# Performance work log

Measured on AMD Instinct MI355X. Metric: run time of the kernel, lower is better.

Reference implementation:

```python
import jax, jax.numpy as jnp
import numpy as np

N = 50000
E = 640000
NFEAT = 128
NHID = 128
ALPHA = 0.2  # leaky relu slope


def setup_inputs() -> dict:
    key = jax.random.key(0)
    k1, k2, k3, k4, k5 = jax.random.split(key, 5)
    x = jax.random.normal(k1, (N, NFEAT), dtype=jnp.float32)
    W = jax.random.normal(k2, (NFEAT, NHID), dtype=jnp.float32) * (1.0 / np.sqrt(NFEAT))
    a = jax.random.normal(k3, (1, 2 * NHID), dtype=jnp.float32) * 0.1
    # every node appears at least once as a source so rowsum > 0 (as in a real adjacency)
    src = jnp.concatenate([jnp.arange(N, dtype=jnp.int64 if jax.config.read('jax_enable_x64') else jnp.int32),
                           jax.random.randint(k4, (E - N,), 0, N)]).astype(jnp.int32)
    dst = jax.random.randint(k5, (E,), 0, N).astype(jnp.int32)
    edge_index = jnp.stack([src, dst], axis=0)
    return {"x": x, "W": W, "a": a, "edge_index": edge_index, "no_need_param": 0}


def reference(x, W, a, edge_index, no_need_param):
    # SpGraphAttentionLayer (concat=False), single head
    h = x @ W                                   # [N, nhid]
    src, dst = edge_index[0], edge_index[1]     # [E]
    nhid = W.shape[1]
    a1, a2 = a[0, :nhid], a[0, nhid:]
    # a @ cat(h[src], h[dst])  ==  h[src]@a1 + h[dst]@a2
    score = h[src] @ a1 + h[dst] @ a2           # [E]
    e = jnp.exp(-jax.nn.leaky_relu(score, ALPHA))
    n = x.shape[0]
    rowsum = jax.ops.segment_sum(e, src, num_segments=n)              # [N]
    h_prime = jax.ops.segment_sum(e[:, None] * h[dst], src, num_segments=n)  # [N, nhid]
    neighborhood_emb = h_prime / (rowsum[:, None] + 1e-16)
    # fused combine: elu(x @ W - neighborhood aggregation)
    mapped_fea = x @ W
    return jax.nn.elu(mapped_fea - neighborhood_emb)
```

## Files before the change

kernel.cpp:

```cpp
#include <hip/hip_runtime.h>
#include <hip/hip_fp16.h>
#include <math.h>

#define NFEAT 128
#define NHID  128
#define ALPHA 0.2f

typedef __attribute__((ext_vector_type(8))) short short8;
typedef __attribute__((ext_vector_type(4))) float f32x4;

__device__ inline unsigned int pack_bf16x2_rn(float x, float y) {
    unsigned int bx = __float_as_uint(x), by = __float_as_uint(y);
    bx += 0x7fffu + ((bx >> 16) & 1u);
    by += 0x7fffu + ((by >> 16) & 1u);
    return (bx >> 16) | (by & 0xffff0000u);
}

union Frag { unsigned int u[4]; uint4 v; short8 s; };

__global__ __launch_bounds__(256) void prep_wt_kernel(
    const float* __restrict__ W, unsigned int* __restrict__ Wtg,
    int* __restrict__ hist, int n)
{
    const int t = threadIdx.x;

    if (blockIdx.x >= 16) {
        const int n4     = n >> 2;
        const int stride = (gridDim.x - 16) << 8;
        int4* h4 = (int4*)hist;
        for (int i = (blockIdx.x - 16) * 256 + t; i < n4; i += stride)
            h4[i] = make_int4(0, 0, 0, 0);
        for (int i = (n4 << 2) + (blockIdx.x - 16) * 256 + t; i < n; i += stride)
            hist[i] = 0;
        return;
    }

    __shared__ float tile[32][33];
    const int kt = blockIdx.x >> 2;
    const int nt = blockIdx.x & 3;

    {
        const int r = t >> 3, c = t & 7;
        const float4 v = *((const float4*)&W[(size_t)(kt * 32 + r) * NHID + nt * 32 + c * 4]);
        tile[r][c * 4 + 0] = v.x; tile[r][c * 4 + 1] = v.y;
        tile[r][c * 4 + 2] = v.z; tile[r][c * 4 + 3] = v.w;
    }
    __syncthreads();

    const int nn = t & 31;
    #pragma unroll
    for (int i = 0; i < 2; ++i) {
        const int kk = (t >> 5) * 2 + i;
        Wtg[(size_t)(nt * 32 + nn) * 64 + kt * 16 + kk] =
            pack_bf16x2_rn(tile[kk * 2][nn], tile[kk * 2 + 1][nn]);
    }
}

__global__ __launch_bounds__(256) void gemm_h_kernel(
    const float* __restrict__ x, const unsigned int* __restrict__ Wtg,
    const float* __restrict__ a, unsigned int* __restrict__ hbu,
    float* __restrict__ s1, float* __restrict__ s2, int n,
    const int* __restrict__ ei, int* __restrict__ hist, int E, int gemm_blocks)
{
    __shared__ unsigned int Wtu[128 * 64];

    const int t = threadIdx.x;

    if (blockIdx.x >= gemm_blocks) {
        const int E4   = E >> 2;
        const int nthr = (gridDim.x - gemm_blocks) << 8;
        const int g    = (blockIdx.x - gemm_blocks) * 256 + t;
        for (int idx = g; idx < E4; idx += nthr) {
            const int4 s4 = ((const int4*)ei)[idx];
            atomicAdd(&hist[s4.x], 1);
            atomicAdd(&hist[s4.y], 1);
            atomicAdd(&hist[s4.z], 1);
            atomicAdd(&hist[s4.w], 1);
        }
        for (int j = (E4 << 2) + g; j < E; j += nthr) atomicAdd(&hist[ei[j]], 1);
        return;
    }

    #pragma unroll
    for (int i = 0; i < 8; ++i) {
        const int u  = i * 256 + t;
        const uint4 v = ((const uint4*)Wtg)[u];
        const int nn = u >> 4, kc = u & 15;
        *((uint4*)&Wtu[nn * 64 + (kc ^ (nn & 15)) * 4]) = v;
    }

    const int w    = t >> 6;
    const int lane = t & 63;
    const int c    = lane & 15;
    const int quad = lane >> 4;

    const int rowbase = blockIdx.x * 64 + w * 16;

    int arow = rowbase + c; if (arow >= n) arow = n - 1;
    const float4* xp = (const float4*)(x + (size_t)arow * NFEAT);
    float4 xv[8];
    #pragma unroll
    for (int s = 0; s < 4; ++s) {
        xv[2 * s]     = xp[s * 8 + quad * 2];
        xv[2 * s + 1] = xp[s * 8 + quad * 2 + 1];
    }

    float a1v[8], a2v[8];
    #pragma unroll
    for (int tt = 0; tt < 8; ++tt) {
        a1v[tt] = a[tt * 16 + c];
        a2v[tt] = a[NHID + tt * 16 + c];
    }

    f32x4 acc[8];
    #pragma unroll
    for (int tt = 0; tt < 8; ++tt) acc[tt] = (f32x4){0.f, 0.f, 0.f, 0.f};

    __syncthreads();

    #pragma unroll
    for (int s = 0; s < 4; ++s) {
        Frag afr;
        afr.u[0] = pack_bf16x2_rn(xv[2 * s].x,     xv[2 * s].y);
        afr.u[1] = pack_bf16x2_rn(xv[2 * s].z,     xv[2 * s].w);
        afr.u[2] = pack_bf16x2_rn(xv[2 * s + 1].x, xv[2 * s + 1].y);
        afr.u[3] = pack_bf16x2_rn(xv[2 * s + 1].z, xv[2 * s + 1].w);
        const int kc = s * 4 + quad;
        #pragma unroll
        for (int tt = 0; tt < 8; ++tt) {
            Frag bfr;
            bfr.v = *((const uint4*)&Wtu[(tt * 16 + c) * 64 + (kc ^ c) * 4]);
            acc[tt] = __builtin_amdgcn_mfma_f32_16x16x32_bf16(
                afr.s, bfr.s, acc[tt], 0, 0, 0);
        }
    }

    #pragma unroll
    for (int r = 0; r < 4; ++r) {
        const int  row = rowbase + quad * 4 + r;
        const bool ok  = (row < n);
        float p1 = 0.f, p2 = 0.f;
        #pragma unroll
        for (int tt = 0; tt < 8; ++tt) {
            const float v = acc[tt][r];
            p1 = fmaf(v, a1v[tt], p1);
            p2 = fmaf(v, a2v[tt], p2);
        }
        if (ok) {
            uint4 pk;
            pk.x = pack_bf16x2_rn(acc[0][r], acc[1][r]);
            pk.y = pack_bf16x2_rn(acc[2][r], acc[3][r]);
            pk.z = pack_bf16x2_rn(acc[4][r], acc[5][r]);
            pk.w = pack_bf16x2_rn(acc[6][r], acc[7][r]);
            *((uint4*)&hbu[(size_t)row * 64 + c * 4]) = pk;
        }
        #pragma unroll
        for (int off = 1; off <= 8; off <<= 1) {
            p1 += __shfl_xor(p1, off, 64);
            p2 += __shfl_xor(p2, off, 64);
        }
        if (ok && c == 0) { s1[row] = p1; s2[row] = p2; }
    }
}

__global__ __launch_bounds__(256) void scan_block_kernel(
    const int* __restrict__ in, int* __restrict__ out, int* __restrict__ bsums, int n)
{
    __shared__ int s[256];
    const int tid = threadIdx.x;
    const int gid = blockIdx.x * 256 + tid;
    const int v = (gid < n) ? in[gid] : 0;
    s[tid] = v;
    __syncthreads();
    #pragma unroll
    for (int off = 1; off < 256; off <<= 1) {
        const int t2 = (tid >= off) ? s[tid - off] : 0;
        __syncthreads();
        s[tid] += t2;
        __syncthreads();
    }
    if (gid < n) out[gid] = s[tid] - v;
    if (tid == 255) bsums[blockIdx.x] = s[255];
}

__global__ __launch_bounds__(256) void scan_add_kernel(
    int* __restrict__ row_ptr, int* __restrict__ cursor,
    const int* __restrict__ bsums, int n, int E, int nb)
{
    __shared__ int s[256];
    const int tid = threadIdx.x;
    s[tid] = (tid < nb) ? bsums[tid] : 0;
    __syncthreads();
    #pragma unroll
    for (int off = 1; off < 256; off <<= 1) {
        const int t2 = (tid >= off) ? s[tid - off] : 0;
        __syncthreads();
        s[tid] += t2;
        __syncthreads();
    }
    const int offset = (blockIdx.x == 0) ? 0 : s[blockIdx.x - 1];
    const int gid = blockIdx.x * 256 + tid;
    if (gid < n) {
        const int v = row_ptr[gid] + offset;
        row_ptr[gid] = v;
        cursor[gid]  = v;
    }
    if (gid == 0) row_ptr[n] = E;
}

__global__ __launch_bounds__(256) void scatter_kernel(
    const int* __restrict__ ei, const float* __restrict__ s1,
    const float* __restrict__ s2, int* __restrict__ cursor,
    unsigned int* __restrict__ erec, int E)
{
    const int j = blockIdx.x * 256 + threadIdx.x;
    if (j >= E) return;
    const int src = ei[j];
    const int dst = ei[E + j];
    float s = s1[src] + s2[dst];
    s = (s > 0.f) ? s : ALPHA * s;
    const float ev = expf(-s);
    const unsigned int evh = (unsigned int)__half_as_ushort(__float2half(ev));
    const int pos = atomicAdd(&cursor[src], 1);
    erec[pos] = ((unsigned int)dst << 16) | evh;
}

__global__ __launch_bounds__(256) void aggregate_kernel(
    const int* __restrict__ row_ptr, const unsigned int* __restrict__ erec,
    const unsigned int* __restrict__ hbu, float* __restrict__ out, int n)
{
    const int node = (blockIdx.x * 256 + threadIdx.x) >> 4;
    const int l    = threadIdx.x & 15;
    if (node >= n) return;

    const int beg = row_ptr[node];
    const int end = row_ptr[node + 1];

    float acc[8];
    #pragma unroll
    for (int i = 0; i < 8; ++i) acc[i] = 0.f;
    float rs = 0.f;

    const uint4* hbu4 = (const uint4*)hbu;

    #define BL(x) __uint_as_float((x) << 16)
    #define BH(x) __uint_as_float((x) & 0xffff0000u)
    #define ACC4(u, ev)                                   \
        acc[0] = fmaf(ev, BL(u.x), acc[0]);               \
        acc[4] = fmaf(ev, BH(u.x), acc[4]);               \
        acc[1] = fmaf(ev, BL(u.y), acc[1]);               \
        acc[5] = fmaf(ev, BH(u.y), acc[5]);               \
        acc[2] = fmaf(ev, BL(u.z), acc[2]);               \
        acc[6] = fmaf(ev, BH(u.z), acc[6]);               \
        acc[3] = fmaf(ev, BL(u.w), acc[3]);               \
        acc[7] = fmaf(ev, BH(u.w), acc[7]);

    int e = beg;
    for (; e + 8 <= end; e += 8) {
        unsigned int rr[8];
        uint4 u[8];
        #pragma unroll
        for (int i = 0; i < 8; ++i) rr[i] = erec[e + i];
        #pragma unroll
        for (int i = 0; i < 8; ++i)
            u[i] = hbu4[(size_t)(rr[i] >> 16) * 16 + l];
        #pragma unroll
        for (int i = 0; i < 8; ++i) {
            const float ev = __half2float(__ushort_as_half((unsigned short)(rr[i] & 0xffffu)));
            ACC4(u[i], ev);
            rs += ev;
        }
    }
    for (; e + 2 <= end; e += 2) {
        const unsigned int r0 = erec[e], r1 = erec[e + 1];
        const uint4 u0 = hbu4[(size_t)(r0 >> 16) * 16 + l];
        const uint4 u1 = hbu4[(size_t)(r1 >> 16) * 16 + l];
        const float e0 = __half2float(__ushort_as_half((unsigned short)(r0 & 0xffffu)));
        const float e1 = __half2float(__ushort_as_half((unsigned short)(r1 & 0xffffu)));
        ACC4(u0, e0); ACC4(u1, e1);
        rs += e0 + e1;
    }
    if (e < end) {
        const unsigned int r0 = erec[e];
        const uint4 u0 = hbu4[(size_t)(r0 >> 16) * 16 + l];
        const float e0 = __half2float(__ushort_as_half((unsigned short)(r0 & 0xffffu)));
        ACC4(u0, e0);
        rs += e0;
    }
    #undef ACC4

    const float rinv = 1.0f / (rs + 1e-16f);
    const uint4 us = hbu4[(size_t)node * 16 + l];
    float* op = out + (size_t)node * NHID + l;
    float z;
    z = BL(us.x) - acc[0] * rinv; op[0]   = (z > 0.f) ? z : (expf(z) - 1.f);
    z = BH(us.x) - acc[4] * rinv; op[16]  = (z > 0.f) ? z : (expf(z) - 1.f);
    z = BL(us.y) - acc[1] * rinv; op[32]  = (z > 0.f) ? z : (expf(z) - 1.f);
    z = BH(us.y) - acc[5] * rinv; op[48]  = (z > 0.f) ? z : (expf(z) - 1.f);
    z = BL(us.z) - acc[2] * rinv; op[64]  = (z > 0.f) ? z : (expf(z) - 1.f);
    z = BH(us.z) - acc[6] * rinv; op[80]  = (z > 0.f) ? z : (expf(z) - 1.f);
    z = BL(us.w) - acc[3] * rinv; op[96]  = (z > 0.f) ? z : (expf(z) - 1.f);
    z = BH(us.w) - acc[7] * rinv; op[112] = (z > 0.f) ? z : (expf(z) - 1.f);
    #undef BL
    #undef BH
}

extern "C" void kernel_launch(void* const* d_in, const int* in_sizes, int n_in,
                              void* d_out, int out_size, void* d_ws, size_t ws_size,
                              hipStream_t stream) {
    const float* x  = (const float*)d_in[0];
    const float* W  = (const float*)d_in[1];
    const float* a  = (const float*)d_in[2];
    const int*   ei = (const int*)d_in[3];

    const int n = in_sizes[0] / NFEAT;
    const int E = in_sizes[3] / 2;
    const int nb = (n + 255) / 256;

    float* out = (float*)d_out;

    unsigned int* hbu    = (unsigned int*)d_ws;
    float*        s1     = (float*)(hbu + (size_t)n * 64);
    float*        s2     = s1 + n;
    unsigned int* erec   = (unsigned int*)(s2 + n);
    unsigned int* Wtg    = erec + E;
    int*          hist   = (int*)(Wtg + 8192);
    int*          bsums  = hist + n;
    int*          row_ptr = bsums + 256;
    int*          cursor  = row_ptr + (n + 1);

    prep_wt_kernel<<<16 + 50, 256, 0, stream>>>(W, Wtg, hist, n);

    const int gemm_blocks = (n + 63) / 64;
    const int hist_blocks = 128;
    gemm_h_kernel<<<gemm_blocks + hist_blocks, 256, 0, stream>>>(
        x, Wtg, a, hbu, s1, s2, n, ei, hist, E, gemm_blocks);

    scan_block_kernel<<<nb, 256, 0, stream>>>(hist, row_ptr, bsums, n);
    scan_add_kernel<<<nb, 256, 0, stream>>>(row_ptr, cursor, bsums, n, E, nb);

    scatter_kernel<<<(E + 255) / 256, 256, 0, stream>>>(ei, s1, s2, cursor, erec, E);

    aggregate_kernel<<<((size_t)n * 16 + 255) / 256, 256, 0, stream>>>(
        row_ptr, erec, hbu, out, n);
}
```

Before: 177.7 us.

## Fuse all stages into one persistent cooperative kernel with grid syncs

Replaces the six separate launches (weight prep, GEMM plus histogram, two scan passes, scatter, aggregate) with a single cooperative persistent kernel. The stages are separated by grid.sync, and each stage uses grid-stride loops over a grid sized from occupancy and capped at 1024 blocks. The scan now uses wave shuffles, and the output uses nontemporal stores. This removes per-launch overhead and idle tails between kernels, but the histogram now runs serially after the GEMM instead of alongside it, every stage is limited to the capped grid, and the 32KB shared buffer may limit occupancy.

```diff
diff --git a/kernel.cpp b/kernel.cpp
--- a/kernel.cpp
+++ b/kernel.cpp
@@ -1,6 +1,9 @@
 #include <hip/hip_runtime.h>
+#include <hip/hip_cooperative_groups.h>
 #include <hip/hip_fp16.h>
 #include <math.h>
+
+namespace cg = cooperative_groups;
 
 #define NFEAT 128
 #define NHID  128
@@ -18,291 +21,301 @@
 
 union Frag { unsigned int u[4]; uint4 v; short8 s; };
 
-__global__ __launch_bounds__(256) void prep_wt_kernel(
-    const float* __restrict__ W, unsigned int* __restrict__ Wtg,
-    int* __restrict__ hist, int n)
+__device__ inline int blk_incl_scan(int v, int* ws) {
+    const int lane = threadIdx.x & 63;
+    const int w    = threadIdx.x >> 6;
+    #pragma unroll
+    for (int off = 1; off < 64; off <<= 1) {
+        const int tv = __shfl_up(v, off, 64);
+        if (lane >= off) v += tv;
+    }
+    if (lane == 63) ws[w] = v;
+    __syncthreads();
+    int add = 0;
+    #pragma unroll
+    for (int i = 0; i < 3; ++i) if (i < w) add += ws[i];
+    __syncthreads();
+    return v + add;
+}
+
+__global__ __launch_bounds__(256) void mega_kernel(
+    const float* __restrict__ x, const float* __restrict__ W,
+    const float* __restrict__ a, const int* __restrict__ ei,
+    float* __restrict__ out, unsigned int* __restrict__ hbu,
+    float* __restrict__ s1, float* __restrict__ s2,
+    unsigned int* __restrict__ erec, unsigned int* __restrict__ Wtg,
+    int* __restrict__ hist, int* __restrict__ bsums,
+    int* __restrict__ row_ptr, int* __restrict__ cursor, int n, int E)
 {
-    const int t = threadIdx.x;
-
-    if (blockIdx.x >= 16) {
-        const int n4     = n >> 2;
-        const int stride = (gridDim.x - 16) << 8;
+    cg::grid_group grid = cg::this_grid();
+    __shared__ unsigned int Wtu[128 * 64];
+
+    const int t        = threadIdx.x;
+    const int gtid     = blockIdx.x * 256 + t;
+    const int nthreads = gridDim.x << 8;
+    const int nb       = (n + 255) >> 8;
+
+    {
+        float (*tile)[33] = (float (*)[33])Wtu;
+        for (int job = blockIdx.x; job < 16; job += gridDim.x) {
+            const int kt = job >> 2, nt = job & 3;
+            __syncthreads();
+            {
+                const int r = t >> 3, cc = t & 7;
+                const float4 v = *((const float4*)&W[(size_t)(kt * 32 + r) * NHID + nt * 32 + cc * 4]);
+                tile[r][cc * 4 + 0] = v.x; tile[r][cc * 4 + 1] = v.y;
+                tile[r][cc * 4 + 2] = v.z; tile[r][cc * 4 + 3] = v.w;
+            }
+            __syncthreads();
+            const int nn = t & 31;
+            #pragma unroll
+            for (int i = 0; i < 2; ++i) {
+                const int kk = (t >> 5) * 2 + i;
+                Wtg[(size_t)(nt * 32 + nn) * 64 + kt * 16 + kk] =
+                    pack_bf16x2_rn(tile[kk * 2][nn], tile[kk * 2 + 1][nn]);
+            }
+        }
+        const int n4 = n >> 2;
         int4* h4 = (int4*)hist;
-        for (int i = (blockIdx.x - 16) * 256 + t; i < n4; i += stride)
-            h4[i] = make_int4(0, 0, 0, 0);
-        for (int i = (n4 << 2) + (blockIdx.x - 16) * 256 + t; i < n; i += stride)
-            hist[i] = 0;
-        return;
-    }
-
-    __shared__ float tile[32][33];
-    const int kt = blockIdx.x >> 2;
-    const int nt = blockIdx.x & 3;
-
-    {
-        const int r = t >> 3, c = t & 7;
-        const float4 v = *((const float4*)&W[(size_t)(kt * 32 + r) * NHID + nt * 32 + c * 4]);
-        tile[r][c * 4 + 0] = v.x; tile[r][c * 4 + 1] = v.y;
-        tile[r][c * 4 + 2] = v.z; tile[r][c * 4 + 3] = v.w;
-    }
-    __syncthreads();
-
-    const int nn = t & 31;
-    #pragma unroll
-    for (int i = 0; i < 2; ++i) {
-        const int kk = (t >> 5) * 2 + i;
-        Wtg[(size_t)(nt * 32 + nn) * 64 + kt * 16 + kk] =
-            pack_bf16x2_rn(tile[kk * 2][nn], tile[kk * 2 + 1][nn]);
-    }
-}
-
-__global__ __launch_bounds__(256) void gemm_h_kernel(
-    const float* __restrict__ x, const unsigned int* __restrict__ Wtg,
-    const float* __restrict__ a, unsigned int* __restrict__ hbu,
-    float* __restrict__ s1, float* __restrict__ s2, int n,
-    const int* __restrict__ ei, int* __restrict__ hist, int E, int gemm_blocks)
-{
-    __shared__ unsigned int Wtu[128 * 64];
-
-    const int t = threadIdx.x;
-
-    if (blockIdx.x >= gemm_blocks) {
-        const int E4   = E >> 2;
-        const int nthr = (gridDim.x - gemm_blocks) << 8;
-        const int g    = (blockIdx.x - gemm_blocks) * 256 + t;
-        for (int idx = g; idx < E4; idx += nthr) {
+        for (int i = gtid; i < n4; i += nthreads) h4[i] = make_int4(0, 0, 0, 0);
+        for (int i = (n4 << 2) + gtid; i < n; i += nthreads) hist[i] = 0;
+    }
+    grid.sync();
+
+    {
+        #pragma unroll
+        for (int i = 0; i < 8; ++i) {
+            const int u  = i * 256 + t;
+            const uint4 v = ((const uint4*)Wtg)[u];
+            const int nn = u >> 4, kc = u & 15;
+            *((uint4*)&Wtu[nn * 64 + (kc ^ (nn & 15)) * 4]) = v;
+        }
+        __syncthreads();
+
+        const int w    = t >> 6;
+        const int lane = t & 63;
+        const int c    = lane & 15;
+        const int quad = lane >> 4;
+
+        float a1v[8], a2v[8];
+        #pragma unroll
+        for (int tt = 0; tt < 8; ++tt) {
+            a1v[tt] = a[tt * 16 + c];
+            a2v[tt] = a[NHID + tt * 16 + c];
+        }
+
+        const int gemm_tiles = (n + 63) >> 6;
+        for (int tb = blockIdx.x; tb < gemm_tiles; tb += gridDim.x) {
+            const int rowbase = tb * 64 + w * 16;
+            int arow = rowbase + c; if (arow >= n) arow = n - 1;
+            const float4* xp = (const float4*)(x + (size_t)arow * NFEAT);
+            float4 xv[8];
+            #pragma unroll
+            for (int s = 0; s < 4; ++s) {
+                xv[2 * s]     = xp[s * 8 + quad * 2];
+                xv[2 * s + 1] = xp[s * 8 + quad * 2 + 1];
+            }
+            f32x4 acc[8];
+            #pragma unroll
+            for (int tt = 0; tt < 8; ++tt) acc[tt] = (f32x4){0.f, 0.f, 0.f, 0.f};
+
+            #pragma unroll
+            for (int s = 0; s < 4; ++s) {
+                Frag afr;
+                afr.u[0] = pack_bf16x2_rn(xv[2 * s].x,     xv[2 * s].y);
+                afr.u[1] = pack_bf16x2_rn(xv[2 * s].z,     xv[2 * s].w);
+                afr.u[2] = pack_bf16x2_rn(xv[2 * s + 1].x, xv[2 * s + 1].y);
+                afr.u[3] = pack_bf16x2_rn(xv[2 * s + 1].z, xv[2 * s + 1].w);
+                const int kc = s * 4 + quad;
+                #pragma unroll
+                for (int tt = 0; tt < 8; ++tt) {
+                    Frag bfr;
+                    bfr.v = *((const uint4*)&Wtu[(tt * 16 + c) * 64 + (kc ^ c) * 4]);
+                    acc[tt] = __builtin_amdgcn_mfma_f32_16x16x32_bf16(
+                        afr.s, bfr.s, acc[tt], 0, 0, 0);
+                }
+            }
+
+            #pragma unroll
+            for (int r = 0; r < 4; ++r) {
+                const int  row = rowbase + quad * 4 + r;
+                const bool ok  = (row < n);
+                float p1 = 0.f, p2 = 0.f;
+                #pragma unroll
+                for (int tt = 0; tt < 8; ++tt) {
+                    const float v = acc[tt][r];
+                    p1 = fmaf(v, a1v[tt], p1);
+                    p2 = fmaf(v, a2v[tt], p2);
+                }
+                if (ok) {
+                    uint4 pk;
+                    pk.x = pack_bf16x2_rn(acc[0][r], acc[1][r]);
+                    pk.y = pack_bf16x2_rn(acc[2][r], acc[3][r]);
+                    pk.z = pack_bf16x2_rn(acc[4][r], acc[5][r]);
+                    pk.w = pack_bf16x2_rn(acc[6][r], acc[7][r]);
+                    *((uint4*)&hbu[(size_t)row * 64 + c * 4]) = pk;
+                }
+                #pragma unroll
+                for (int off = 1; off <= 8; off <<= 1) {
+                    p1 += __shfl_xor(p1, off, 64);
+                    p2 += __shfl_xor(p2, off, 64);
+                }
+                if (ok && c == 0) { s1[row] = p1; s2[row] = p2; }
+            }
+        }
+
+        const int E4 = E >> 2;
+        for (int idx = gtid; idx < E4; idx += nthreads) {
             const int4 s4 = ((const int4*)ei)[idx];
             atomicAdd(&hist[s4.x], 1);
             atomicAdd(&hist[s4.y], 1);
             atomicAdd(&hist[s4.z], 1);
             atomicAdd(&hist[s4.w], 1);
         }
-        for (int j = (E4 << 2) + g; j < E; j += nthr) atomicAdd(&hist[ei[j]], 1);
-        return;
-    }
-
-    #pragma unroll
-    for (int i = 0; i < 8; ++i) {
-        const int u  = i * 256 + t;
-        const uint4 v = ((const uint4*)Wtg)[u];
-        const int nn = u >> 4, kc = u & 15;
-        *((uint4*)&Wtu[nn * 64 + (kc ^ (nn & 15)) * 4]) = v;
-    }
-
-    const int w    = t >> 6;
-    const int lane = t & 63;
-    const int c    = lane & 15;
-    const int quad = lane >> 4;
-
-    const int rowbase = blockIdx.x * 64 + w * 16;
-
-    int arow = rowbase + c; if (arow >= n) arow = n - 1;
-    const float4* xp = (const float4*)(x + (size_t)arow * NFEAT);
-    float4 xv[8];
-    #pragma unroll
-    for (int s = 0; s < 4; ++s) {
-        xv[2 * s]     = xp[s * 8 + quad * 2];
-        xv[2 * s + 1] = xp[s * 8 + quad * 2 + 1];
-    }
-
-    float a1v[8], a2v[8];
-    #pragma unroll
-    for (int tt = 0; tt < 8; ++tt) {
-        a1v[tt] = a[tt * 16 + c];
-        a2v[tt] = a[NHID + tt * 16 + c];
-    }
-
-    f32x4 acc[8];
-    #pragma unroll
-    for (int tt = 0; tt < 8; ++tt) acc[tt] = (f32x4){0.f, 0.f, 0.f, 0.f};
-
-    __syncthreads();
-
-    #pragma unroll
-    for (int s = 0; s < 4; ++s) {
-        Frag afr;
-        afr.u[0] = pack_bf16x2_rn(xv[2 * s].x,     xv[2 * s].y);
-        afr.u[1] = pack_bf16x2_rn(xv[2 * s].z,     xv[2 * s].w);
-        afr.u[2] = pack_bf16x2_rn(xv[2 * s + 1].x, xv[2 * s + 1].y);
-        afr.u[3] = pack_bf16x2_rn(xv[2 * s + 1].z, xv[2 * s + 1].w);
-        const int kc = s * 4 + quad;
-        #pragma unroll
-        for (int tt = 0; tt < 8; ++tt) {
-            Frag bfr;
-            bfr.v = *((const uint4*)&Wtu[(tt * 16 + c) * 64 + (kc ^ c) * 4]);
-            acc[tt] = __builtin_amdgcn_mfma_f32_16x16x32_bf16(
-                afr.s, bfr.s, acc[tt], 0, 0, 0);
-        }
-    }
-
-    #pragma unroll
-    for (int r = 0; r < 4; ++r) {
-        const int  row = rowbase + quad * 4 + r;
-        const bool ok  = (row < n);
-        float p1 = 0.f, p2 = 0.f;
-        #pragma unroll
-        for (int tt = 0; tt < 8; ++tt) {
-            const float v = acc[tt][r];
-            p1 = fmaf(v, a1v[tt], p1);
-            p2 = fmaf(v, a2v[tt], p2);
-        }
-        if (ok) {
-            uint4 pk;
-            pk.x = pack_bf16x2_rn(acc[0][r], acc[1][r]);
-            pk.y = pack_bf16x2_rn(acc[2][r], acc[3][r]);
-            pk.z = pack_bf16x2_rn(acc[4][r], acc[5][r]);
-            pk.w = pack_bf16x2_rn(acc[6][r], acc[7][r]);
-            *((uint4*)&hbu[(size_t)row * 64 + c * 4]) = pk;
-        }
-        #pragma unroll
-        for (int off = 1; off <= 8; off <<= 1) {
-            p1 += __shfl_xor(p1, off, 64);
-            p2 += __shfl_xor(p2, off, 64);
-        }
-        if (ok && c == 0) { s1[row] = p1; s2[row] = p2; }
-    }
-}
-
-__global__ __launch_bounds__(256) void scan_block_kernel(
-    const int* __restrict__ in, int* __restrict__ out, int* __restrict__ bsums, int n)
-{
-    __shared__ int s[256];
-    const int tid = threadIdx.x;
-    const int gid = blockIdx.x * 256 + tid;
-    const int v = (gid < n) ? in[gid] : 0;
-    s[tid] = v;
-    __syncthreads();
-    #pragma unroll
-    for (int off = 1; off < 256; off <<= 1) {
-        const int t2 = (tid >= off) ? s[tid - off] : 0;
-        __syncthreads();
-        s[tid] += t2;
-        __syncthreads();
-    }
-    if (gid < n) out[gid] = s[tid] - v;
-    if (tid == 255) bsums[blockIdx.x] = s[255];
-}
-
-__global__ __launch_bounds__(256) void scan_add_kernel(
-    int* __restrict__ row_ptr, int* __restrict__ cursor,
-    const int* __restrict__ bsums, int n, int E, int nb)
-{
-    __shared__ int s[256];
-    const int tid = threadIdx.x;
-    s[tid] = (tid < nb) ? bsums[tid] : 0;
-    __syncthreads();
-    #pragma unroll
-    for (int off = 1; off < 256; off <<= 1) {
-        const int t2 = (tid >= off) ? s[tid - off] : 0;
-        __syncthreads();
-        s[tid] += t2;
-        __syncthreads();
-    }
-    const int offset = (blockIdx.x == 0) ? 0 : s[blockIdx.x - 1];
-    const int gid = blockIdx.x * 256 + tid;
-    if (gid < n) {
-        const int v = row_ptr[gid] + offset;
-        row_ptr[gid] = v;
-        cursor[gid]  = v;
-    }
-    if (gid == 0) row_ptr[n] = E;
-}
-
-__global__ __launch_bounds__(256) void scatter_kernel(
-    const int* __restrict__ ei, const float* __restrict__ s1,
-    const float* __restrict__ s2, int* __restrict__ cursor,
-    unsigned int* __restrict__ erec, int E)
-{
-    const int j = blockIdx.x * 256 + threadIdx.x;
-    if (j >= E) return;
-    const int src = ei[j];
-    const int dst = ei[E + j];
-    float s = s1[src] + s2[dst];
-    s = (s > 0.f) ? s : ALPHA * s;
-    const float ev = expf(-s);
-    const unsigned int evh = (unsigned int)__half_as_ushort(__float2half(ev));
-    const int pos = atomicAdd(&cursor[src], 1);
-    erec[pos] = ((unsigned int)dst << 16) | evh;
-}
-
-__global__ __launch_bounds__(256) void aggregate_kernel(
-    const int* __restrict__ row_ptr, const unsigned int* __restrict__ erec,
-    const unsigned int* __restrict__ hbu, float* __restrict__ out, int n)
-{
-    const int node = (blockIdx.x * 256 + threadIdx.x) >> 4;
-    const int l    = threadIdx.x & 15;
-    if (node >= n) return;
-
-    const int beg = row_ptr[node];
-    const int end = row_ptr[node + 1];
-
-    float acc[8];
-    #pragma unroll
-    for (int i = 0; i < 8; ++i) acc[i] = 0.f;
-    float rs = 0.f;
-
-    const uint4* hbu4 = (const uint4*)hbu;
-
-    #define BL(x) __uint_as_float((x) << 16)
-    #define BH(x) __uint_as_float((x) & 0xffff0000u)
-    #define ACC4(u, ev)                                   \
-        acc[0] = fmaf(ev, BL(u.x), acc[0]);               \
-        acc[4] = fmaf(ev, BH(u.x), acc[4]);               \
-        acc[1] = fmaf(ev, BL(u.y), acc[1]);               \
-        acc[5] = fmaf(ev, BH(u.y), acc[5]);               \
-        acc[2] = fmaf(ev, BL(u.z), acc[2]);               \
-        acc[6] = fmaf(ev, BH(u.z), acc[6]);               \
-        acc[3] = fmaf(ev, BL(u.w), acc[3]);               \
-        acc[7] = fmaf(ev, BH(u.w), acc[7]);
-
-    int e = beg;
-    for (; e + 8 <= end; e += 8) {
-        unsigned int rr[8];
-        uint4 u[8];
-        #pragma unroll
-        for (int i = 0; i < 8; ++i) rr[i] = erec[e + i];
-        #pragma unroll
-        for (int i = 0; i < 8; ++i)
-            u[i] = hbu4[(size_t)(rr[i] >> 16) * 16 + l];
-        #pragma unroll
-        for (int i = 0; i < 8; ++i) {
-            const float ev = __half2float(__ushort_as_half((unsigned short)(rr[i] & 0xffffu)));
-            ACC4(u[i], ev);
-            rs += ev;
-        }
-    }
-    for (; e + 2 <= end; e += 2) {
-        const unsigned int r0 = erec[e], r1 = erec[e + 1];
-        const uint4 u0 = hbu4[(size_t)(r0 >> 16) * 16 + l];
-        const uint4 u1 = hbu4[(size_t)(r1 >> 16) * 16 + l];
-        const float e0 = __half2float(__ushort_as_half((unsigned short)(r0 & 0xffffu)));
-        const float e1 = __half2float(__ushort_as_half((unsigned short)(r1 & 0xffffu)));
-        ACC4(u0, e0); ACC4(u1, e1);
-        rs += e0 + e1;
-    }
-    if (e < end) {
-        const unsigned int r0 = erec[e];
-        const uint4 u0 = hbu4[(size_t)(r0 >> 16) * 16 + l];
-        const float e0 = __half2float(__ushort_as_half((unsigned short)(r0 & 0xffffu)));
-        ACC4(u0, e0);
-        rs += e0;
-    }
-    #undef ACC4
-
-    const float rinv = 1.0f / (rs + 1e-16f);
-    const uint4 us = hbu4[(size_t)node * 16 + l];
-    float* op = out + (size_t)node * NHID + l;
-    float z;
-    z = BL(us.x) - acc[0] * rinv; op[0]   = (z > 0.f) ? z : (expf(z) - 1.f);
-    z = BH(us.x) - acc[4] * rinv; op[16]  = (z > 0.f) ? z : (expf(z) - 1.f);
-    z = BL(us.y) - acc[1] * rinv; op[32]  = (z > 0.f) ? z : (expf(z) - 1.f);
-    z = BH(us.y) - acc[5] * rinv; op[48]  = (z > 0.f) ? z : (expf(z) - 1.f);
-    z = BL(us.z) - acc[2] * rinv; op[64]  = (z > 0.f) ? z : (expf(z) - 1.f);
-    z = BH(us.z) - acc[6] * rinv; op[80]  = (z > 0.f) ? z : (expf(z) - 1.f);
-    z = BL(us.w) - acc[3] * rinv; op[96]  = (z > 0.f) ? z : (expf(z) - 1.f);
-    z = BH(us.w) - acc[7] * rinv; op[112] = (z > 0.f) ? z : (expf(z) - 1.f);
-    #undef BL
-    #undef BH
+        for (int j = (E4 << 2) + gtid; j < E; j += nthreads) atomicAdd(&hist[ei[j]], 1);
+    }
+    grid.sync();
+
+    {
+        int* ws = (int*)Wtu;
+        for (int tb = blockIdx.x; tb < nb; tb += gridDim.x) {
+            const int gid = tb * 256 + t;
+            const int v   = (gid < n) ? hist[gid] : 0;
+            const int inc = blk_incl_scan(v, ws);
+            if (gid < n) row_ptr[gid] = inc - v;
+            if (t == 255) bsums[tb] = inc;
+        }
+    }
+    grid.sync();
+
+    if (blockIdx.x == 0) {
+        int* ws = (int*)Wtu;
+        const int v   = (t < nb) ? bsums[t] : 0;
+        const int inc = blk_incl_scan(v, ws);
+        bsums[t] = inc;
+    }
+    grid.sync();
+
+    {
+        for (int tb = blockIdx.x; tb < nb; tb += gridDim.x) {
+            const int gid = tb * 256 + t;
+            if (gid < n) {
+                const int off = tb ? bsums[tb - 1] : 0;
+                const int v = row_ptr[gid] + off;
+                row_ptr[gid] = v;
+                cursor[gid]  = v;
+            }
+        }
+        if (gtid == 0) row_ptr[n] = E;
+    }
+    grid.sync();
+
+    {
+        const int E4 = E >> 2;
+        for (int i = gtid; i < E4; i += nthreads) {
+            const int4 s4 = ((const int4*)ei)[i];
+            const int4 d4 = ((const int4*)(ei + E))[i];
+            const int sa[4] = { s4.x, s4.y, s4.z, s4.w };
+            const int da[4] = { d4.x, d4.y, d4.z, d4.w };
+            #pragma unroll
+            for (int k = 0; k < 4; ++k) {
+                float s = s1[sa[k]] + s2[da[k]];
+                s = (s > 0.f) ? s : ALPHA * s;
+                const float ev = expf(-s);
+                const unsigned int evh = (unsigned int)__half_as_ushort(__float2half(ev));
+                const int pos = atomicAdd(&cursor[sa[k]], 1);
+                erec[pos] = ((unsigned int)da[k] << 16) | evh;
+            }
+        }
+        for (int j = (E4 << 2) + gtid; j < E; j += nthreads) {
+            const int src = ei[j];
+            const int dst = ei[E + j];
+            float s = s1[src] + s2[dst];
+            s = (s > 0.f) ? s : ALPHA * s;
+            const float ev = expf(-s);
+            const unsigned int evh = (unsigned int)__half_as_ushort(__float2half(ev));
+            const int pos = atomicAdd(&cursor[src], 1);
+            erec[pos] = ((unsigned int)dst << 16) | evh;
+        }
+    }
+    grid.sync();
+
+    {
+        const uint4* hbu4 = (const uint4*)hbu;
+        const int l   = t & 15;
+        const int gpp = gridDim.x << 4;
+
+        for (int node = gtid >> 4; node < n; node += gpp) {
+            const int beg = row_ptr[node];
+            const int end = row_ptr[node + 1];
+
+            float acc[8];
+            #pragma unroll
+            for (int i = 0; i < 8; ++i) acc[i] = 0.f;
+            float rs = 0.f;
+
+            #define BL(u_) __uint_as_float((u_) << 16)
+            #define BH(u_) __uint_as_float((u_) & 0xffff0000u)
+            #define ACC4(u_, ev_)                               \
+                acc[0] = fmaf(ev_, BL(u_.x), acc[0]);           \
+                acc[4] = fmaf(ev_, BH(u_.x), acc[4]);           \
+                acc[1] = fmaf(ev_, BL(u_.y), acc[1]);           \
+                acc[5] = fmaf(ev_, BH(u_.y), acc[5]);           \
+                acc[2] = fmaf(ev_, BL(u_.z), acc[2]);           \
+                acc[6] = fmaf(ev_, BH(u_.z), acc[6]);           \
+                acc[3] = fmaf(ev_, BL(u_.w), acc[3]);           \
+                acc[7] = fmaf(ev_, BH(u_.w), acc[7]);
+
+            int e = beg;
+            for (; e + 8 <= end; e += 8) {
+                unsigned int rr[8];
+                uint4 u[8];
+                #pragma unroll
+                for (int i = 0; i < 8; ++i) rr[i] = erec[e + i];
+                #pragma unroll
+                for (int i = 0; i < 8; ++i)
+                    u[i] = hbu4[(size_t)(rr[i] >> 16) * 16 + l];
+                #pragma unroll
+                for (int i = 0; i < 8; ++i) {
+                    const float ev = __half2float(__ushort_as_half((unsigned short)(rr[i] & 0xffffu)));
+                    ACC4(u[i], ev);
+                    rs += ev;
+                }
+            }
+            for (; e + 2 <= end; e += 2) {
+                const unsigned int r0 = erec[e], r1 = erec[e + 1];
+                const uint4 u0 = hbu4[(size_t)(r0 >> 16) * 16 + l];
+                const uint4 u1 = hbu4[(size_t)(r1 >> 16) * 16 + l];
+                const float e0 = __half2float(__ushort_as_half((unsigned short)(r0 & 0xffffu)));
+                const float e1 = __half2float(__ushort_as_half((unsigned short)(r1 & 0xffffu)));
+                ACC4(u0, e0); ACC4(u1, e1);
+                rs += e0 + e1;
+            }
+            if (e < end) {
+                const unsigned int r0 = erec[e];
+                const uint4 u0 = hbu4[(size_t)(r0 >> 16) * 16 + l];
+                const float e0 = __half2float(__ushort_as_half((unsigned short)(r0 & 0xffffu)));
+                ACC4(u0, e0);
+                rs += e0;
+            }
+            #undef ACC4
+
+            const float rinv = 1.0f / (rs + 1e-16f);
+            const uint4 us = hbu4[(size_t)node * 16 + l];
+            float* op = out + (size_t)node * NHID + l;
+            float z;
+            z = BL(us.x) - acc[0] * rinv; __builtin_nontemporal_store((z > 0.f) ? z : (expf(z) - 1.f), op);
+            z = BH(us.x) - acc[4] * rinv; __builtin_nontemporal_store((z > 0.f) ? z : (expf(z) - 1.f), op + 16);
+            z = BL(us.y) - acc[1] * rinv; __builtin_nontemporal_store((z > 0.f) ? z : (expf(z) - 1.f), op + 32);
+            z = BH(us.y) - acc[5] * rinv; __builtin_nontemporal_store((z > 0.f) ? z : (expf(z) - 1.f), op + 48);
+            z = BL(us.z) - acc[2] * rinv; __builtin_nontemporal_store((z > 0.f) ? z : (expf(z) - 1.f), op + 64);
+            z = BH(us.z) - acc[6] * rinv; __builtin_nontemporal_store((z > 0.f) ? z : (expf(z) - 1.f), op + 80);
+            z = BL(us.w) - acc[3] * rinv; __builtin_nontemporal_store((z > 0.f) ? z : (expf(z) - 1.f), op + 96);
+            z = BH(us.w) - acc[7] * rinv; __builtin_nontemporal_store((z > 0.f) ? z : (expf(z) - 1.f), op + 112);
+            #undef BL
+            #undef BH
+        }
+    }
 }
 
 extern "C" void kernel_launch(void* const* d_in, const int* in_sizes, int n_in,
@@ -313,9 +326,8 @@
     const float* a  = (const float*)d_in[2];
     const int*   ei = (const int*)d_in[3];
 
-    const int n = in_sizes[0] / NFEAT;
-    const int E = in_sizes[3] / 2;
-    const int nb = (n + 255) / 256;
+    int n = in_sizes[0] / NFEAT;
+    int E = in_sizes[3] / 2;
 
     float* out = (float*)d_out;
 
@@ -329,18 +341,19 @@
     int*          row_ptr = bsums + 256;
     int*          cursor  = row_ptr + (n + 1);
 
-    prep_wt_kernel<<<16 + 50, 256, 0, stream>>>(W, Wtg, hist, n);
-
-    const int gemm_blocks = (n + 63) / 64;
-    const int hist_blocks = 128;
-    gemm_h_kernel<<<gemm_blocks + hist_blocks, 256, 0, stream>>>(
-        x, Wtg, a, hbu, s1, s2, n, ei, hist, E, gemm_blocks);
-
-    scan_block_kernel<<<nb, 256, 0, stream>>>(hist, row_ptr, bsums, n);
-    scan_add_kernel<<<nb, 256, 0, stream>>>(row_ptr, cursor, bsums, n, E, nb);
-
-    scatter_kernel<<<(E + 255) / 256, 256, 0, stream>>>(ei, s1, s2, cursor, erec, E);
-
-    aggregate_kernel<<<((size_t)n * 16 + 255) / 256, 256, 0, stream>>>(
-        row_ptr, erec, hbu, out, n);
+    static int s_grid = 0;
+    if (s_grid == 0) {
+        int occ = 0;
+        if (hipOccupancyMaxActiveBlocksPerMultiprocessor(&occ, mega_kernel, 256, 0) != hipSuccess || occ < 1)
+            occ = 2;
+        long g = (long)occ * 256;
+        if (g > 1024) g = 1024;
+        s_grid = (int)g;
+    }
+
+    void* args[] = { (void*)&x, (void*)&W, (void*)&a, (void*)&ei, (void*)&out,
+                     (void*)&hbu, (void*)&s1, (void*)&s2, (void*)&erec, (void*)&Wtg,
+                     (void*)&hist, (void*)&bsums, (void*)&row_ptr, (void*)&cursor,
+                     (void*)&n, (void*)&E };
+    hipLaunchCooperativeKernel(mega_kernel, dim3(s_grid), dim3(256), args, 0, stream);
 }
```

Measured after the change: 386.4 us. 2.17x slower.
